# Kernel optimization log

Hardware: AMD Instinct MI355X
Metric: run time of the kernel (lower is better)

The kernel has to match this reference:

```python
import jax, jax.numpy as jnp
import numpy as np

N = 100000
E = 3200000
C = 128
POOL_RATIO = 0.5
N_REGIONS = 360
N_GRAPHS = 64


def setup_inputs() -> dict:
    key = jax.random.key(0)
    k_x, k_ei, k_ea, k_r, k_b, k_w, k_bias = jax.random.split(key, 7)
    x = jax.random.normal(k_x, (N, C), dtype=jnp.float32)
    edge_index = jax.random.randint(k_ei, (2, E), 0, N, dtype=jnp.int64)
    edge_attr = jax.random.normal(k_ea, (E,), dtype=jnp.float32)
    region_indices = jax.random.randint(k_r, (N,), 0, N_REGIONS, dtype=jnp.int64)
    batch = jnp.sort(jax.random.randint(k_b, (N,), 0, N_GRAPHS, dtype=jnp.int64))
    # nn.Linear(in_channels, 1): weight [1, C], bias [1]; store as [C, 1] for x @ W
    bound = 1.0 / np.sqrt(C)
    W = jax.random.uniform(k_w, (C, 1), dtype=jnp.float32, minval=-bound, maxval=bound)
    b = jax.random.uniform(k_bias, (1,), dtype=jnp.float32, minval=-bound, maxval=bound)
    return {"x": x, "edge_index": edge_index, "edge_attr": edge_attr,
            "region_indices": region_indices, "batch": batch, "W": W, "b": b}


def reference(x, edge_index, edge_attr, region_indices, batch, W, b):
    num_nodes = x.shape[0]
    # scores = Linear(x).squeeze() -> [N]
    scores = (x @ W + b)[:, 0]
    k = max(int(num_nodes * POOL_RATIO), 1)  # static
    _, topk_indices = jax.lax.top_k(scores, k)  # same node set as torch topk(sorted=False)
    x_pooled = x[topk_indices]                       # [k, C]
    region_indices_pooled = region_indices[topk_indices]
    batch_pooled = batch[topk_indices]
    # boolean keep-mask over nodes
    mask = jnp.zeros((num_nodes,), dtype=bool).at[topk_indices].set(True)
    # edge filtering: keep edges whose both endpoints survive
    edge_mask = mask[edge_index[0]] & mask[edge_index[1]]  # [E]
    # jit-compatible compaction: stable-sort valid edges to the front, pad tail
    order = jnp.argsort(~edge_mask, stable=True)
    edge_mask_sorted = edge_mask[order]
    edge_index_f = jnp.where(edge_mask_sorted[None, :], edge_index[:, order], -1)
    edge_attr_f = jnp.where(edge_mask_sorted, edge_attr[order], 0.0)
    num_edges_kept = edge_mask.sum()  # number of valid leading entries
    return (x_pooled, edge_index_f, edge_attr_f, region_indices_pooled,
            batch_pooled, scores, num_edges_kept)
```

## Files before the change

kernel.cpp:

```cpp
#include <hip/hip_runtime.h>

#define NNODES 100000
#define NEDGES 3200000
#define CH     128
#define KPOOL  50000
#define NBUCK  (1 << 17)
#define BUCK_SCALE 8192.0

#define OFF_X   0
#define OFF_EI  6400000
#define OFF_EA  12800000
#define OFF_REG 16000000
#define OFF_BAT 16050000
#define OFF_SC  16100000
#define OFF_NE  16200000

#define NB_EDGE 3125

__device__ __forceinline__ int bucketOf(double s) {
    double u = (8.0 - s) * BUCK_SCALE;
    int b = (int)u;
    if (b < 0) b = 0;
    if (b > NBUCK - 1) b = NBUCK - 1;
    return b;
}

__global__ void k_scores(const float* __restrict__ x, const float* __restrict__ W,
                         const float* __restrict__ bias, double* __restrict__ score_d,
                         float* __restrict__ out, unsigned* __restrict__ hist) {
    int row  = blockIdx.x * 4 + (threadIdx.x >> 6);
    int lane = threadIdx.x & 63;
    if (row >= NNODES) return;
    int c = lane * 2;
    float2 xv = *(const float2*)(x + (size_t)row * CH + c);
    double acc = (double)xv.x * (double)W[c] + (double)xv.y * (double)W[c + 1];
    for (int off = 32; off > 0; off >>= 1) acc += __shfl_down(acc, off, 64);
    if (lane == 0) {
        double s = acc + (double)bias[0];
        score_d[row] = s;
        out[OFF_SC + row] = (float)s;
        atomicAdd(&hist[bucketOf(s)], 1u);
    }
}

__global__ void k_scan1(const unsigned* __restrict__ hist, unsigned* __restrict__ bbase,
                        unsigned* __restrict__ spart) {
    int t = threadIdx.x, blk = blockIdx.x;
    int i0 = blk * 1024 + t * 4;
    uint4 h = *(const uint4*)(hist + i0);
    unsigned s = h.x + h.y + h.z + h.w;
    __shared__ unsigned sc[256];
    sc[t] = s; __syncthreads();
    for (int off = 1; off < 256; off <<= 1) {
        unsigned v = (t >= off) ? sc[t - off] : 0u;
        __syncthreads(); sc[t] += v; __syncthreads();
    }
    unsigned excl = sc[t] - s;
    if (t == 255) spart[blk] = sc[255];
    uint4 o; o.x = excl; o.y = o.x + h.x; o.z = o.y + h.y; o.w = o.z + h.z;
    *(uint4*)(bbase + i0) = o;
}

__global__ void k_scan2(unsigned* __restrict__ spart) {
    int t = threadIdx.x;
    __shared__ unsigned sc[128];
    unsigned v0 = spart[t];
    sc[t] = v0; __syncthreads();
    for (int off = 1; off < 128; off <<= 1) {
        unsigned v = (t >= off) ? sc[t - off] : 0u;
        __syncthreads(); sc[t] += v; __syncthreads();
    }
    spart[t] = sc[t] - v0;
}

__global__ void k_scatter(const double* __restrict__ score_d, const unsigned* __restrict__ bbase,
                          const unsigned* __restrict__ spart, unsigned* __restrict__ bcnt,
                          unsigned* __restrict__ elems) {
    int i = blockIdx.x * 256 + threadIdx.x;
    if (i >= NNODES) return;
    int b = bucketOf(score_d[i]);
    unsigned base = bbase[b] + spart[b >> 10];
    unsigned slot = base + atomicAdd(&bcnt[b], 1u);
    elems[slot] = i;
}

__global__ void k_rank(const double* __restrict__ score_d, const unsigned* __restrict__ bbase,
                       const unsigned* __restrict__ spart, const unsigned* __restrict__ hist,
                       const unsigned* __restrict__ elems, unsigned* __restrict__ perm,
                       unsigned* __restrict__ kb) {
    int i = blockIdx.x * 256 + threadIdx.x;
    if (i >= NNODES) return;
    double s = score_d[i];
    int b = bucketOf(s);
    unsigned st = bbase[b] + spart[b >> 10], c = hist[b];
    unsigned r = st;
    if (c > 1) {
        for (unsigned m = 0; m < c; ++m) {
            unsigned j = elems[st + m];
            if (j == (unsigned)i) continue;
            double sj = score_d[j];
            if (sj > s || (sj == s && j < (unsigned)i)) r++;
        }
    }
    perm[r] = (unsigned)i;
    if (r < KPOOL) atomicOr(&kb[i >> 5], 1u << (i & 31));
}

__global__ void k_pool(const float* __restrict__ x, const int* __restrict__ region,
                       const int* __restrict__ batch, const unsigned* __restrict__ perm,
                       float* __restrict__ out) {
    int r    = blockIdx.x * 4 + (threadIdx.x >> 6);
    int lane = threadIdx.x & 63;
    if (r >= KPOOL) return;
    unsigned i = perm[r];
    float2 v = *(const float2*)(x + (size_t)i * CH + lane * 2);
    *(float2*)(out + OFF_X + (size_t)r * CH + lane * 2) = v;
    if (lane == 0) {
        out[OFF_REG + r] = (float)region[i];
        out[OFF_BAT + r] = (float)batch[i];
    }
}

__global__ void k_ecount(const int* __restrict__ ei, const unsigned* __restrict__ kb,
                         unsigned* __restrict__ epart) {
    int t = threadIdx.x, blk = blockIdx.x;
    size_t e0 = (size_t)blk * 1024 + (size_t)t * 4;
    int4 a = *(const int4*)(ei + e0);
    int4 b = *(const int4*)(ei + NEDGES + e0);
    unsigned c = 0;
    c += (kb[a.x >> 5] >> (a.x & 31)) & (kb[b.x >> 5] >> (b.x & 31)) & 1u;
    c += (kb[a.y >> 5] >> (a.y & 31)) & (kb[b.y >> 5] >> (b.y & 31)) & 1u;
    c += (kb[a.z >> 5] >> (a.z & 31)) & (kb[b.z >> 5] >> (b.z & 31)) & 1u;
    c += (kb[a.w >> 5] >> (a.w & 31)) & (kb[b.w >> 5] >> (b.w & 31)) & 1u;
    __shared__ unsigned sc[256];
    sc[t] = c; __syncthreads();
    for (int off = 128; off > 0; off >>= 1) {
        if (t < off) sc[t] += sc[t + off];
        __syncthreads();
    }
    if (t == 0) epart[blk] = sc[0];
}

__global__ void k_escan(const unsigned* __restrict__ epart, unsigned* __restrict__ epartx,
                        int* __restrict__ ntotal, float* __restrict__ out) {
    int t = threadIdx.x;
    unsigned v[4]; unsigned s = 0;
    for (int q = 0; q < 4; ++q) { int i = t * 4 + q; v[q] = (i < NB_EDGE) ? epart[i] : 0u; s += v[q]; }
    __shared__ unsigned sc[1024];
    sc[t] = s; __syncthreads();
    for (int off = 1; off < 1024; off <<= 1) {
        unsigned w = (t >= off) ? sc[t - off] : 0u;
        __syncthreads(); sc[t] += w; __syncthreads();
    }
    unsigned excl = sc[t] - s;
    for (int q = 0; q < 4; ++q) { int i = t * 4 + q; if (i < NB_EDGE) epartx[i] = excl; excl += v[q]; }
    if (t == 1023) { *ntotal = (int)sc[1023]; out[OFF_NE] = (float)sc[1023]; }
}

__global__ void k_escatter(const int* __restrict__ ei, const float* __restrict__ attr,
                           const unsigned* __restrict__ kb, const unsigned* __restrict__ epartx,
                           const int* __restrict__ ntotal, float* __restrict__ out) {
    int t = threadIdx.x, blk = blockIdx.x;
    size_t e0 = (size_t)blk * 1024 + (size_t)t * 4;
    int4 a = *(const int4*)(ei + e0);
    int4 b = *(const int4*)(ei + NEDGES + e0);
    float4 at = *(const float4*)(attr + e0);
    unsigned m0 = (kb[a.x >> 5] >> (a.x & 31)) & (kb[b.x >> 5] >> (b.x & 31)) & 1u;
    unsigned m1 = (kb[a.y >> 5] >> (a.y & 31)) & (kb[b.y >> 5] >> (b.y & 31)) & 1u;
    unsigned m2 = (kb[a.z >> 5] >> (a.z & 31)) & (kb[b.z >> 5] >> (b.z & 31)) & 1u;
    unsigned m3 = (kb[a.w >> 5] >> (a.w & 31)) & (kb[b.w >> 5] >> (b.w & 31)) & 1u;
    unsigned cnt = m0 + m1 + m2 + m3;
    __shared__ unsigned sc[256];
    __shared__ float sA[1024], sB[1024], sT[1024];
    sc[t] = cnt; __syncthreads();
    for (int off = 1; off < 256; off <<= 1) {
        unsigned w = (t >= off) ? sc[t - off] : 0u;
        __syncthreads(); sc[t] += w; __syncthreads();
    }
    unsigned p = sc[t] - cnt;
    if (m0) { sA[p] = (float)a.x; sB[p] = (float)b.x; sT[p] = at.x; p++; }
    if (m1) { sA[p] = (float)a.y; sB[p] = (float)b.y; sT[p] = at.y; p++; }
    if (m2) { sA[p] = (float)a.z; sB[p] = (float)b.z; sT[p] = at.z; p++; }
    if (m3) { sA[p] = (float)a.w; sB[p] = (float)b.w; sT[p] = at.w; p++; }
    __syncthreads();
    unsigned cntAll = sc[255];
    unsigned base = epartx[blk];
    for (unsigned u = t; u < cntAll; u += 256) {
        out[OFF_EI + base + u]          = sA[u];
        out[OFF_EI + NEDGES + base + u] = sB[u];
        out[OFF_EA + base + u]          = sT[u];
    }
    int total = *ntotal;
    size_t tlen = (size_t)NEDGES - (size_t)total;
    size_t chunk = (tlen + NB_EDGE - 1) / NB_EDGE;
    size_t s0 = (size_t)total + (size_t)blk * chunk;
    size_t s1 = s0 + chunk; if (s1 > (size_t)NEDGES) s1 = (size_t)NEDGES;
    for (size_t q = s0 + (size_t)t; q < s1; q += 256) {
        out[OFF_EI + q]          = -1.0f;
        out[OFF_EI + NEDGES + q] = -1.0f;
        out[OFF_EA + q]          = 0.0f;
    }
}

extern "C" void kernel_launch(void* const* d_in, const int* in_sizes, int n_in,
                              void* d_out, int out_size, void* d_ws, size_t ws_size,
                              hipStream_t stream) {
    const float* x      = (const float*)d_in[0];
    const int*   ei     = (const int*)d_in[1];
    const float* attr   = (const float*)d_in[2];
    const int*   region = (const int*)d_in[3];
    const int*   batch  = (const int*)d_in[4];
    const float* W      = (const float*)d_in[5];
    const float* bias   = (const float*)d_in[6];
    float* out = (float*)d_out;

    char* ws = (char*)d_ws;
    double*   score_d = (double*)(ws + 0);
    unsigned* hist    = (unsigned*)(ws + 800000);
    unsigned* bcnt    = (unsigned*)(ws + 1324288);
    unsigned* kb      = (unsigned*)(ws + 1848576);
    unsigned* bbase   = (unsigned*)(ws + 1861120);
    unsigned* elems   = (unsigned*)(ws + 2385408);
    unsigned* perm    = (unsigned*)(ws + 2785408);
    unsigned* spart   = (unsigned*)(ws + 3185408);
    unsigned* epart   = (unsigned*)(ws + 3185920);
    unsigned* epartx  = (unsigned*)(ws + 3198432);
    int*      ntotal  = (int*)(ws + 3210944);

    (void)hipMemsetAsync(ws + 800000, 0, 1061120, stream);

    k_scores  <<<NNODES / 4, 256, 0, stream>>>(x, W, bias, score_d, out, hist);
    k_scan1   <<<NBUCK / 1024, 256, 0, stream>>>(hist, bbase, spart);
    k_scan2   <<<1, 128, 0, stream>>>(spart);
    k_scatter <<<(NNODES + 255) / 256, 256, 0, stream>>>(score_d, bbase, spart, bcnt, elems);
    k_rank    <<<(NNODES + 255) / 256, 256, 0, stream>>>(score_d, bbase, spart, hist, elems, perm, kb);
    k_pool    <<<KPOOL / 4, 256, 0, stream>>>(x, region, batch, perm, out);
    k_ecount  <<<NB_EDGE, 256, 0, stream>>>(ei, kb, epart);
    k_escan   <<<1, 1024, 0, stream>>>(epart, epartx, ntotal, out);
    k_escatter<<<NB_EDGE, 256, 0, stream>>>(ei, attr, kb, epartx, ntotal, out);
}
```

Measured before the change: 99.42 us.

## Use decoupled lookback scans and fuse pool, edge count and scatter into fewer launches

Replaces the two-pass bucket scan and the three-kernel edge count/scan/scatter with single-pass decoupled-lookback scans that use ticketed block ordering. The edge tail fill (-1 indices, 0 attributes) is written up front inside the scores kernel, and compaction later overwrites the head. Pool gathering shares a launch with edge compaction, the memset becomes a small init kernel, and the per-bucket counter array goes away by atomically incrementing bbase. This cuts launches and removes a full second pass over the edge list. In exchange it adds spin-waiting, and writes the edge region twice.

```diff
diff --git a/kernel.cpp b/kernel.cpp
--- a/kernel.cpp
+++ b/kernel.cpp
@@ -15,7 +15,24 @@
 #define OFF_SC  16100000
 #define OFF_NE  16200000
 
-#define NB_EDGE 3125
+#define NB_EDGE   3125
+#define SCORE_BLK 25000
+#define FILL_BLK  2344
+#define POOL_BLK  12500
+
+#define WS_SCORE   0
+#define WS_HIST    800000
+#define WS_KB      1324288
+#define WS_SSTATE  1336832
+#define WS_ESTATE  1337856
+#define WS_TICKETS 1362856
+#define WS_BBASE   1362864
+#define WS_ELEMS   1887152
+#define WS_PERM    2287152
+#define ZERO_U4    35179
+
+#define AGGBIT (1ULL << 62)
+#define INCBIT (1ULL << 63)
 
 __device__ __forceinline__ int bucketOf(double s) {
     double u = (8.0 - s) * BUCK_SCALE;
@@ -25,74 +42,107 @@
     return b;
 }
 
-__global__ void k_scores(const float* __restrict__ x, const float* __restrict__ W,
-                         const float* __restrict__ bias, double* __restrict__ score_d,
-                         float* __restrict__ out, unsigned* __restrict__ hist) {
-    int row  = blockIdx.x * 4 + (threadIdx.x >> 6);
-    int lane = threadIdx.x & 63;
-    if (row >= NNODES) return;
-    int c = lane * 2;
-    float2 xv = *(const float2*)(x + (size_t)row * CH + c);
-    double acc = (double)xv.x * (double)W[c] + (double)xv.y * (double)W[c + 1];
-    for (int off = 32; off > 0; off >>= 1) acc += __shfl_down(acc, off, 64);
-    if (lane == 0) {
-        double s = acc + (double)bias[0];
-        score_d[row] = s;
-        out[OFF_SC + row] = (float)s;
-        atomicAdd(&hist[bucketOf(s)], 1u);
-    }
-}
-
-__global__ void k_scan1(const unsigned* __restrict__ hist, unsigned* __restrict__ bbase,
-                        unsigned* __restrict__ spart) {
-    int t = threadIdx.x, blk = blockIdx.x;
-    int i0 = blk * 1024 + t * 4;
+__device__ __forceinline__ unsigned lookback(unsigned long long* state, unsigned blk,
+                                             unsigned total) {
+    unsigned prefix = 0;
+    if (blk == 0) {
+        atomicExch(&state[0], INCBIT | (unsigned long long)total);
+    } else {
+        atomicExch(&state[blk], AGGBIT | (unsigned long long)total);
+        int j = (int)blk - 1;
+        for (;;) {
+            unsigned long long v;
+            do {
+                v = atomicAdd(&state[j], 0ULL);
+                if (!(v >> 62)) __builtin_amdgcn_s_sleep(4);
+            } while (!(v >> 62));
+            prefix += (unsigned)v;
+            if (v & INCBIT) break;
+            --j;
+        }
+        atomicExch(&state[blk], INCBIT | (unsigned long long)(prefix + total));
+    }
+    return prefix;
+}
+
+__global__ void k_init(uint4* __restrict__ z) {
+    int idx = blockIdx.x * 256 + threadIdx.x;
+    if (idx < ZERO_U4) z[idx] = make_uint4(0u, 0u, 0u, 0u);
+}
+
+__global__ void k_scores_fill(const float* __restrict__ x, const float* __restrict__ W,
+                              const float* __restrict__ bias, double* __restrict__ score_d,
+                              float* __restrict__ out, unsigned* __restrict__ hist) {
+    int bid = blockIdx.x, tid = threadIdx.x;
+    if (bid < SCORE_BLK) {
+        int row  = bid * 4 + (tid >> 6);
+        int lane = tid & 63;
+        int c = lane * 2;
+        float2 xv = *(const float2*)(x + (size_t)row * CH + c);
+        double acc = (double)xv.x * (double)W[c] + (double)xv.y * (double)W[c + 1];
+        for (int off = 32; off > 0; off >>= 1) acc += __shfl_down(acc, off, 64);
+        if (lane == 0) {
+            double s = acc + (double)bias[0];
+            score_d[row] = s;
+            out[OFF_SC + row] = (float)s;
+            atomicAdd(&hist[bucketOf(s)], 1u);
+        }
+    } else {
+        int fb = bid - SCORE_BLK;
+        float4* dst = (float4*)(out + OFF_EI);
+        const float4 neg = make_float4(-1.f, -1.f, -1.f, -1.f);
+        const float4 zer = make_float4(0.f, 0.f, 0.f, 0.f);
+#pragma unroll
+        for (int q = 0; q < 4; ++q) {
+            int f = fb * 1024 + q * 256 + tid;
+            if (f < 2400000) dst[f] = (f < 1600000) ? neg : zer;
+        }
+    }
+}
+
+__global__ void k_scan_lb(const unsigned* __restrict__ hist, unsigned* __restrict__ bbase,
+                          unsigned long long* __restrict__ sstate, unsigned* __restrict__ tickets) {
+    __shared__ unsigned stkt, sprefix;
+    __shared__ unsigned sc[256];
+    int t = threadIdx.x;
+    if (t == 0) stkt = atomicAdd(&tickets[0], 1u);
+    __syncthreads();
+    unsigned blk = stkt;
+    int i0 = (int)blk * 1024 + t * 4;
     uint4 h = *(const uint4*)(hist + i0);
     unsigned s = h.x + h.y + h.z + h.w;
-    __shared__ unsigned sc[256];
     sc[t] = s; __syncthreads();
     for (int off = 1; off < 256; off <<= 1) {
         unsigned v = (t >= off) ? sc[t - off] : 0u;
         __syncthreads(); sc[t] += v; __syncthreads();
     }
     unsigned excl = sc[t] - s;
-    if (t == 255) spart[blk] = sc[255];
-    uint4 o; o.x = excl; o.y = o.x + h.x; o.z = o.y + h.y; o.w = o.z + h.z;
+    unsigned tot  = sc[255];
+    if (t == 0) sprefix = lookback(sstate, blk, tot);
+    __syncthreads();
+    unsigned base = sprefix + excl;
+    uint4 o; o.x = base; o.y = o.x + h.x; o.z = o.y + h.y; o.w = o.z + h.z;
     *(uint4*)(bbase + i0) = o;
 }
 
-__global__ void k_scan2(unsigned* __restrict__ spart) {
-    int t = threadIdx.x;
-    __shared__ unsigned sc[128];
-    unsigned v0 = spart[t];
-    sc[t] = v0; __syncthreads();
-    for (int off = 1; off < 128; off <<= 1) {
-        unsigned v = (t >= off) ? sc[t - off] : 0u;
-        __syncthreads(); sc[t] += v; __syncthreads();
-    }
-    spart[t] = sc[t] - v0;
-}
-
-__global__ void k_scatter(const double* __restrict__ score_d, const unsigned* __restrict__ bbase,
-                          const unsigned* __restrict__ spart, unsigned* __restrict__ bcnt,
+__global__ void k_scatter(const double* __restrict__ score_d, unsigned* __restrict__ bbase,
                           unsigned* __restrict__ elems) {
     int i = blockIdx.x * 256 + threadIdx.x;
     if (i >= NNODES) return;
     int b = bucketOf(score_d[i]);
-    unsigned base = bbase[b] + spart[b >> 10];
-    unsigned slot = base + atomicAdd(&bcnt[b], 1u);
+    unsigned slot = atomicAdd(&bbase[b], 1u);
     elems[slot] = i;
 }
 
 __global__ void k_rank(const double* __restrict__ score_d, const unsigned* __restrict__ bbase,
-                       const unsigned* __restrict__ spart, const unsigned* __restrict__ hist,
-                       const unsigned* __restrict__ elems, unsigned* __restrict__ perm,
-                       unsigned* __restrict__ kb) {
+                       const unsigned* __restrict__ hist, const unsigned* __restrict__ elems,
+                       unsigned* __restrict__ perm, unsigned* __restrict__ kb) {
     int i = blockIdx.x * 256 + threadIdx.x;
     if (i >= NNODES) return;
     double s = score_d[i];
     int b = bucketOf(s);
-    unsigned st = bbase[b] + spart[b >> 10], c = hist[b];
+    unsigned c = hist[b];
+    unsigned st = bbase[b] - c;
     unsigned r = st;
     if (c > 1) {
         for (unsigned m = 0; m < c; ++m) {
@@ -106,62 +156,31 @@
     if (r < KPOOL) atomicOr(&kb[i >> 5], 1u << (i & 31));
 }
 
-__global__ void k_pool(const float* __restrict__ x, const int* __restrict__ region,
-                       const int* __restrict__ batch, const unsigned* __restrict__ perm,
-                       float* __restrict__ out) {
-    int r    = blockIdx.x * 4 + (threadIdx.x >> 6);
-    int lane = threadIdx.x & 63;
-    if (r >= KPOOL) return;
-    unsigned i = perm[r];
-    float2 v = *(const float2*)(x + (size_t)i * CH + lane * 2);
-    *(float2*)(out + OFF_X + (size_t)r * CH + lane * 2) = v;
-    if (lane == 0) {
-        out[OFF_REG + r] = (float)region[i];
-        out[OFF_BAT + r] = (float)batch[i];
-    }
-}
-
-__global__ void k_ecount(const int* __restrict__ ei, const unsigned* __restrict__ kb,
-                         unsigned* __restrict__ epart) {
-    int t = threadIdx.x, blk = blockIdx.x;
-    size_t e0 = (size_t)blk * 1024 + (size_t)t * 4;
-    int4 a = *(const int4*)(ei + e0);
-    int4 b = *(const int4*)(ei + NEDGES + e0);
-    unsigned c = 0;
-    c += (kb[a.x >> 5] >> (a.x & 31)) & (kb[b.x >> 5] >> (b.x & 31)) & 1u;
-    c += (kb[a.y >> 5] >> (a.y & 31)) & (kb[b.y >> 5] >> (b.y & 31)) & 1u;
-    c += (kb[a.z >> 5] >> (a.z & 31)) & (kb[b.z >> 5] >> (b.z & 31)) & 1u;
-    c += (kb[a.w >> 5] >> (a.w & 31)) & (kb[b.w >> 5] >> (b.w & 31)) & 1u;
+__global__ void k_poolesc(const float* __restrict__ x, const int* __restrict__ region,
+                          const int* __restrict__ batch, const unsigned* __restrict__ perm,
+                          const int* __restrict__ ei, const float* __restrict__ attr,
+                          const unsigned* __restrict__ kb, unsigned long long* __restrict__ estate,
+                          unsigned* __restrict__ tickets, float* __restrict__ out) {
+    int tid = threadIdx.x;
+    if (blockIdx.x < POOL_BLK) {
+        int r    = blockIdx.x * 4 + (tid >> 6);
+        int lane = tid & 63;
+        unsigned i = perm[r];
+        float2 v = *(const float2*)(x + (size_t)i * CH + lane * 2);
+        *(float2*)(out + OFF_X + (size_t)r * CH + lane * 2) = v;
+        if (lane == 0) {
+            out[OFF_REG + r] = (float)region[i];
+            out[OFF_BAT + r] = (float)batch[i];
+        }
+        return;
+    }
+    __shared__ unsigned stkt, sbase;
     __shared__ unsigned sc[256];
-    sc[t] = c; __syncthreads();
-    for (int off = 128; off > 0; off >>= 1) {
-        if (t < off) sc[t] += sc[t + off];
-        __syncthreads();
-    }
-    if (t == 0) epart[blk] = sc[0];
-}
-
-__global__ void k_escan(const unsigned* __restrict__ epart, unsigned* __restrict__ epartx,
-                        int* __restrict__ ntotal, float* __restrict__ out) {
-    int t = threadIdx.x;
-    unsigned v[4]; unsigned s = 0;
-    for (int q = 0; q < 4; ++q) { int i = t * 4 + q; v[q] = (i < NB_EDGE) ? epart[i] : 0u; s += v[q]; }
-    __shared__ unsigned sc[1024];
-    sc[t] = s; __syncthreads();
-    for (int off = 1; off < 1024; off <<= 1) {
-        unsigned w = (t >= off) ? sc[t - off] : 0u;
-        __syncthreads(); sc[t] += w; __syncthreads();
-    }
-    unsigned excl = sc[t] - s;
-    for (int q = 0; q < 4; ++q) { int i = t * 4 + q; if (i < NB_EDGE) epartx[i] = excl; excl += v[q]; }
-    if (t == 1023) { *ntotal = (int)sc[1023]; out[OFF_NE] = (float)sc[1023]; }
-}
-
-__global__ void k_escatter(const int* __restrict__ ei, const float* __restrict__ attr,
-                           const unsigned* __restrict__ kb, const unsigned* __restrict__ epartx,
-                           const int* __restrict__ ntotal, float* __restrict__ out) {
-    int t = threadIdx.x, blk = blockIdx.x;
-    size_t e0 = (size_t)blk * 1024 + (size_t)t * 4;
+    __shared__ float sA[1024], sB[1024], sT[1024];
+    if (tid == 0) stkt = atomicAdd(&tickets[1], 1u);
+    __syncthreads();
+    unsigned blk = stkt;
+    size_t e0 = (size_t)blk * 1024 + (size_t)tid * 4;
     int4 a = *(const int4*)(ei + e0);
     int4 b = *(const int4*)(ei + NEDGES + e0);
     float4 at = *(const float4*)(attr + e0);
@@ -170,35 +189,28 @@
     unsigned m2 = (kb[a.z >> 5] >> (a.z & 31)) & (kb[b.z >> 5] >> (b.z & 31)) & 1u;
     unsigned m3 = (kb[a.w >> 5] >> (a.w & 31)) & (kb[b.w >> 5] >> (b.w & 31)) & 1u;
     unsigned cnt = m0 + m1 + m2 + m3;
-    __shared__ unsigned sc[256];
-    __shared__ float sA[1024], sB[1024], sT[1024];
-    sc[t] = cnt; __syncthreads();
+    sc[tid] = cnt; __syncthreads();
     for (int off = 1; off < 256; off <<= 1) {
-        unsigned w = (t >= off) ? sc[t - off] : 0u;
-        __syncthreads(); sc[t] += w; __syncthreads();
-    }
-    unsigned p = sc[t] - cnt;
+        unsigned w = (tid >= off) ? sc[tid - off] : 0u;
+        __syncthreads(); sc[tid] += w; __syncthreads();
+    }
+    unsigned p = sc[tid] - cnt;
+    unsigned cntAll = sc[255];
+    if (tid == 0) {
+        unsigned prefix = lookback(estate, blk, cntAll);
+        sbase = prefix;
+        if (blk == NB_EDGE - 1) out[OFF_NE] = (float)(prefix + cntAll);
+    }
     if (m0) { sA[p] = (float)a.x; sB[p] = (float)b.x; sT[p] = at.x; p++; }
     if (m1) { sA[p] = (float)a.y; sB[p] = (float)b.y; sT[p] = at.y; p++; }
     if (m2) { sA[p] = (float)a.z; sB[p] = (float)b.z; sT[p] = at.z; p++; }
     if (m3) { sA[p] = (float)a.w; sB[p] = (float)b.w; sT[p] = at.w; p++; }
     __syncthreads();
-    unsigned cntAll = sc[255];
-    unsigned base = epartx[blk];
-    for (unsigned u = t; u < cntAll; u += 256) {
+    unsigned base = sbase;
+    for (unsigned u = tid; u < cntAll; u += 256) {
         out[OFF_EI + base + u]          = sA[u];
         out[OFF_EI + NEDGES + base + u] = sB[u];
         out[OFF_EA + base + u]          = sT[u];
-    }
-    int total = *ntotal;
-    size_t tlen = (size_t)NEDGES - (size_t)total;
-    size_t chunk = (tlen + NB_EDGE - 1) / NB_EDGE;
-    size_t s0 = (size_t)total + (size_t)blk * chunk;
-    size_t s1 = s0 + chunk; if (s1 > (size_t)NEDGES) s1 = (size_t)NEDGES;
-    for (size_t q = s0 + (size_t)t; q < s1; q += 256) {
-        out[OFF_EI + q]          = -1.0f;
-        out[OFF_EI + NEDGES + q] = -1.0f;
-        out[OFF_EA + q]          = 0.0f;
     }
 }
 
@@ -215,27 +227,21 @@
     float* out = (float*)d_out;
 
     char* ws = (char*)d_ws;
-    double*   score_d = (double*)(ws + 0);
-    unsigned* hist    = (unsigned*)(ws + 800000);
-    unsigned* bcnt    = (unsigned*)(ws + 1324288);
-    unsigned* kb      = (unsigned*)(ws + 1848576);
-    unsigned* bbase   = (unsigned*)(ws + 1861120);
-    unsigned* elems   = (unsigned*)(ws + 2385408);
-    unsigned* perm    = (unsigned*)(ws + 2785408);
-    unsigned* spart   = (unsigned*)(ws + 3185408);
-    unsigned* epart   = (unsigned*)(ws + 3185920);
-    unsigned* epartx  = (unsigned*)(ws + 3198432);
-    int*      ntotal  = (int*)(ws + 3210944);
-
-    (void)hipMemsetAsync(ws + 800000, 0, 1061120, stream);
-
-    k_scores  <<<NNODES / 4, 256, 0, stream>>>(x, W, bias, score_d, out, hist);
-    k_scan1   <<<NBUCK / 1024, 256, 0, stream>>>(hist, bbase, spart);
-    k_scan2   <<<1, 128, 0, stream>>>(spart);
-    k_scatter <<<(NNODES + 255) / 256, 256, 0, stream>>>(score_d, bbase, spart, bcnt, elems);
-    k_rank    <<<(NNODES + 255) / 256, 256, 0, stream>>>(score_d, bbase, spart, hist, elems, perm, kb);
-    k_pool    <<<KPOOL / 4, 256, 0, stream>>>(x, region, batch, perm, out);
-    k_ecount  <<<NB_EDGE, 256, 0, stream>>>(ei, kb, epart);
-    k_escan   <<<1, 1024, 0, stream>>>(epart, epartx, ntotal, out);
-    k_escatter<<<NB_EDGE, 256, 0, stream>>>(ei, attr, kb, epartx, ntotal, out);
-}
+    double*             score_d = (double*)(ws + WS_SCORE);
+    unsigned*           hist    = (unsigned*)(ws + WS_HIST);
+    unsigned*           kb      = (unsigned*)(ws + WS_KB);
+    unsigned long long* sstate  = (unsigned long long*)(ws + WS_SSTATE);
+    unsigned long long* estate  = (unsigned long long*)(ws + WS_ESTATE);
+    unsigned*           tickets = (unsigned*)(ws + WS_TICKETS);
+    unsigned*           bbase   = (unsigned*)(ws + WS_BBASE);
+    unsigned*           elems   = (unsigned*)(ws + WS_ELEMS);
+    unsigned*           perm    = (unsigned*)(ws + WS_PERM);
+
+    k_init       <<<(ZERO_U4 + 255) / 256, 256, 0, stream>>>((uint4*)(ws + WS_HIST));
+    k_scores_fill<<<SCORE_BLK + FILL_BLK, 256, 0, stream>>>(x, W, bias, score_d, out, hist);
+    k_scan_lb    <<<NBUCK / 1024, 256, 0, stream>>>(hist, bbase, sstate, tickets);
+    k_scatter    <<<(NNODES + 255) / 256, 256, 0, stream>>>(score_d, bbase, elems);
+    k_rank       <<<(NNODES + 255) / 256, 256, 0, stream>>>(score_d, bbase, hist, elems, perm, kb);
+    k_poolesc    <<<POOL_BLK + NB_EDGE, 256, 0, stream>>>(x, region, batch, perm, ei, attr,
+                                                          kb, estate, tickets, out);
+}
```

After: 145.8 us. 46.6% more time.
